# Optimization experiments

Measured on AMD Instinct MI355X. Metric: run time of the kernel, lower is better.

Reference implementation:

```python
import jax, jax.numpy as jnp
import numpy as np

N_FEATURES = 256
HIDDEN = 16
BATCH = 32768


def setup_inputs() -> dict:
    key = jax.random.key(0)
    ks = jax.random.split(key, 8)
    F, H = N_FEATURES, HIDDEN
    x = jax.random.normal(ks[0], (BATCH, F), dtype=jnp.float32)
    # Stacked per-feature subnet params (torch Linear: y = x @ W.T + b)
    s1 = 1.0  # fan_in=1 for fc1
    W1 = jax.random.uniform(ks[1], (F, H), minval=-s1, maxval=s1, dtype=jnp.float32)
    b1 = jax.random.uniform(ks[2], (F, H), minval=-s1, maxval=s1, dtype=jnp.float32)
    s2 = 1.0 / np.sqrt(H)
    W2 = jax.random.uniform(ks[3], (F, H, H), minval=-s2, maxval=s2, dtype=jnp.float32)  # [F, out, in]
    b2 = jax.random.uniform(ks[4], (F, H), minval=-s2, maxval=s2, dtype=jnp.float32)
    W3 = jax.random.uniform(ks[5], (F, H), minval=-s2, maxval=s2, dtype=jnp.float32)  # out=1
    b3 = jax.random.uniform(ks[6], (F,), minval=-s2, maxval=s2, dtype=jnp.float32)
    linear_a = jnp.zeros((F,), dtype=jnp.float32)
    bias_b = jnp.zeros((1,), dtype=jnp.float32)
    return {"x": x, "linear_a": linear_a, "bias_b": bias_b,
            "W1": W1, "b1": b1, "W2": W2, "b2": b2, "W3": W3, "b3": b3}


def reference(x, linear_a, bias_b, W1, b1, W2, b2, W3, b3):
    # lin term: (x * a).sum(1)
    lin = x @ linear_a  # [B]
    # all subnets batched: h1 [B, F, H]
    h1 = jax.nn.relu(x[:, :, None] * W1[None, :, :] + b1[None, :, :])
    # fc2: y = h1 @ W2.T per feature; W2 is [F, out, in]
    h2 = jax.nn.relu(jnp.einsum('bfh,fkh->bfk', h1, W2) + b2[None, :, :])
    # fc3 -> scalar per feature, then sum over features
    out_f = jnp.einsum('bfh,fh->bf', h2, W3) + b3[None, :]  # [B, F]
    add_sum = out_f.sum(axis=1)  # [B]
    logits = lin + bias_b[0] + add_sum
    return logits
```

## Files before the change

### kernel.cpp

```cpp
#include <hip/hip_runtime.h>


typedef float    f32x4 __attribute__((ext_vector_type(4)));
typedef _Float16 f16x4 __attribute__((ext_vector_type(4)));
typedef __fp16   pk16x2 __attribute__((ext_vector_type(2)));

__device__ __forceinline__ f16x4 cvt4(f32x4 v) {
    pk16x2 lo = __builtin_amdgcn_cvt_pkrtz(v[0], v[1]);
    pk16x2 hi = __builtin_amdgcn_cvt_pkrtz(v[2], v[3]);
    union { unsigned u[2]; f16x4 h; } un;
    un.u[0] = __builtin_bit_cast(unsigned, lo);
    un.u[1] = __builtin_bit_cast(unsigned, hi);
    return un.h;
}

__device__ __forceinline__ f16x4 relu_h(f16x4 v) {
    f16x4 z = {};
    return __builtin_elementwise_max(v, z);
}

__device__ __forceinline__ f32x4 relu_f(f32x4 v) {
    f32x4 z = {0.f, 0.f, 0.f, 0.f};
    return __builtin_elementwise_max(v, z);
}

#define FCHUNK 16
#define XR     20
#define W2R    20
#define BATCH  32768

__global__ __launch_bounds__(256) void igann_kernel(
    const float* __restrict__ x,  const float* __restrict__ la,
    const float* __restrict__ bb, const float* __restrict__ W1,
    const float* __restrict__ b1, const float* __restrict__ W2,
    const float* __restrict__ b2, const float* __restrict__ W3,
    const float* __restrict__ b3, float* __restrict__ ws)
{
    const int tid = threadIdx.x;
    const int l   = tid & 63;
    const int w   = tid >> 6;
    const int r   = l & 15;
    const int g   = l >> 4;
    const int g4  = g * 4;

    const int rb = blockIdx.x >> 4;
    const int fg = blockIdx.x & 15;
    const int f0 = fg * FCHUNK;
    const int rowbase = rb * 256;

    __shared__ _Float16 xs [256 * XR];
    __shared__ _Float16 w2s[FCHUNK * 16 * W2R];
    __shared__ _Float16 wbs[FCHUNK * 4 * 8];
    __shared__ float2   bws[FCHUNK * 16];
    __shared__ float    sums[256];

    {
        const int rr = tid >> 2;
        const int c4 = (tid & 3) * 4;
        #pragma unroll
        for (int it = 0; it < 4; ++it) {
            const int row = it * 64 + rr;
            f32x4 v = *(const f32x4*)(x + (size_t)(rowbase + row) * 256 + f0 + c4);
            *(f16x4*)(xs + row * XR + c4) = cvt4(v);
        }
    }
    {
        const int f = tid >> 4, n = tid & 15;
        const float* src = W2 + ((size_t)(f0 + f) * 16 + n) * 16;
        _Float16* dst = w2s + (f * 16 + n) * W2R;
        #pragma unroll
        for (int q = 0; q < 4; ++q) {
            f32x4 v = *(const f32x4*)(src + q * 4);
            *(f16x4*)(dst + q * 4) = cvt4(v);
        }
    }
    {
        const int f = tid >> 4, k = tid & 15;
        const int base = f * 32 + (k >> 2) * 8 + (k & 3);
        wbs[base]     = (_Float16)W1[(size_t)(f0 + f) * 16 + k];
        wbs[base + 4] = (_Float16)b1[(size_t)(f0 + f) * 16 + k];
    }
    {
        const int f = tid >> 4, n = tid & 15;
        bws[tid] = make_float2(b2[(size_t)(f0 + f) * 16 + n],
                               W3[(size_t)(f0 + f) * 16 + n]);
    }
    __syncthreads();

    const _Float16* xw = xs + (w * 64 + r) * XR;

    f32x4 acc[4];
    #pragma unroll
    for (int t = 0; t < 4; ++t) acc[t] = (f32x4){0.f, 0.f, 0.f, 0.f};

    for (int fi = 0; fi < FCHUNK; fi += 4) {
        f16x4 xv[4];
        #pragma unroll
        for (int t = 0; t < 4; ++t)
            xv[t] = *(const f16x4*)(xw + t * 16 * XR + fi);

        #pragma unroll
        for (int u = 0; u < 4; ++u) {
            const int f = fi + u;
            f16x4 w1h   = *(const f16x4*)(wbs + f * 32 + g * 8);
            f16x4 b1h   = *(const f16x4*)(wbs + f * 32 + g * 8 + 4);
            f16x4 bfrag = *(const f16x4*)(w2s + (f * 16 + r) * W2R + g4);
            const float2 bw = bws[f * 16 + r];
            const f32x4 cinit = {bw.x, bw.x, bw.x, bw.x};
            const f32x4 w3k4  = {bw.y, bw.y, bw.y, bw.y};

            #pragma unroll
            for (int t = 0; t < 4; ++t) {
                const _Float16 s = xv[t][u];
                f16x4 xb = {s, s, s, s};
                f16x4 h = relu_h(xb * w1h + b1h);
                f32x4 d = __builtin_amdgcn_mfma_f32_16x16x16f16(h, bfrag, cinit, 0, 0, 0);
                acc[t] += relu_f(d) * w3k4;
            }
        }
    }

    #pragma unroll
    for (int t = 0; t < 4; ++t)
        #pragma unroll
        for (int j = 0; j < 4; ++j) {
            float v = acc[t][j];
            v += __shfl_xor(v, 1, 64);
            v += __shfl_xor(v, 2, 64);
            v += __shfl_xor(v, 4, 64);
            v += __shfl_xor(v, 8, 64);
            if (r == 0)
                sums[w * 64 + t * 16 + g4 + j] = v;
        }
    __syncthreads();

    float b3s = 0.f;
    #pragma unroll
    for (int c = 0; c < FCHUNK; ++c) b3s += b3[f0 + c];
    float lin = 0.f;
    const _Float16* xrow = xs + tid * XR;
    #pragma unroll
    for (int c = 0; c < FCHUNK; ++c)
        lin = fmaf((float)xrow[c], la[f0 + c], lin);
    ws[(size_t)fg * BATCH + rowbase + tid] = sums[tid] + lin + b3s;
}

__global__ __launch_bounds__(256) void igann_reduce(
    const float* __restrict__ ws, const float* __restrict__ bb,
    float* __restrict__ out)
{
    const int i = blockIdx.x * 256 + threadIdx.x;
    float s = bb[0];
    #pragma unroll
    for (int gq = 0; gq < 16; ++gq)
        s += ws[(size_t)gq * BATCH + i];
    out[i] = s;
}

extern "C" void kernel_launch(void* const* d_in, const int* in_sizes, int n_in,
                              void* d_out, int out_size, void* d_ws, size_t ws_size,
                              hipStream_t stream) {
    const float* x  = (const float*)d_in[0];
    const float* la = (const float*)d_in[1];
    const float* bb = (const float*)d_in[2];
    const float* W1 = (const float*)d_in[3];
    const float* b1 = (const float*)d_in[4];
    const float* W2 = (const float*)d_in[5];
    const float* b2 = (const float*)d_in[6];
    const float* W3 = (const float*)d_in[7];
    const float* b3 = (const float*)d_in[8];
    float* out = (float*)d_out;
    float* ws  = (float*)d_ws;

    dim3 grid(2048), block(256);
    hipLaunchKernelGGL(igann_kernel, grid, block, 0, stream,
                       x, la, bb, W1, b1, W2, b2, W3, b3, ws);
    hipLaunchKernelGGL(igann_reduce, dim3(128), block, 0, stream,
                       ws, bb, out);
}
```

Measured before the change: 109.2 us.

## Swizzle LDS layouts, alias scratch buffers, and raise occupancy hint

Drops the padded shared-memory rows for x and W2 and uses an XOR swizzle on 4-element groups to avoid bank conflicts. This shrinks LDS use so more blocks fit per CU. The W1/b1 scratch is aliased with the reduction sums buffer, guarded by an added barrier. The launch bounds now ask for 8 waves-per-EU occupancy, and the accumulate uses an explicit FMA. The risks are extra address arithmetic and register pressure under the tighter occupancy bound.

```diff
diff --git a/kernel.cpp b/kernel.cpp
--- a/kernel.cpp
+++ b/kernel.cpp
@@ -25,11 +25,9 @@
 }
 
 #define FCHUNK 16
-#define XR     20
-#define W2R    20
 #define BATCH  32768
 
-__global__ __launch_bounds__(256) void igann_kernel(
+__global__ __launch_bounds__(256, 8) void igann_kernel(
     const float* __restrict__ x,  const float* __restrict__ la,
     const float* __restrict__ bb, const float* __restrict__ W1,
     const float* __restrict__ b1, const float* __restrict__ W2,
@@ -48,30 +46,33 @@
     const int f0 = fg * FCHUNK;
     const int rowbase = rb * 256;
 
-    __shared__ _Float16 xs [256 * XR];
-    __shared__ _Float16 w2s[FCHUNK * 16 * W2R];
-    __shared__ _Float16 wbs[FCHUNK * 4 * 8];
+    __shared__ _Float16 xs [256 * 16];
+    __shared__ _Float16 w2s[FCHUNK * 16 * 16];
+    __shared__ float    wbs_sums[256];
     __shared__ float2   bws[FCHUNK * 16];
-    __shared__ float    sums[256];
+    _Float16* wbs = (_Float16*)wbs_sums;
+    float*    sums = wbs_sums;
 
     {
-        const int rr = tid >> 2;
-        const int c4 = (tid & 3) * 4;
+        const int rr  = tid >> 2;
+        const int c4g = tid & 3;
+        const int sw  = (rr >> 2) & 3;
         #pragma unroll
         for (int it = 0; it < 4; ++it) {
             const int row = it * 64 + rr;
-            f32x4 v = *(const f32x4*)(x + (size_t)(rowbase + row) * 256 + f0 + c4);
-            *(f16x4*)(xs + row * XR + c4) = cvt4(v);
+            f32x4 v = *(const f32x4*)(x + (size_t)(rowbase + row) * 256 + f0 + c4g * 4);
+            *(f16x4*)(xs + row * 16 + ((c4g ^ sw) & 3) * 4) = cvt4(v);
         }
     }
     {
         const int f = tid >> 4, n = tid & 15;
+        const int sw = (n >> 2) & 3;
         const float* src = W2 + ((size_t)(f0 + f) * 16 + n) * 16;
-        _Float16* dst = w2s + (f * 16 + n) * W2R;
+        _Float16* dst = w2s + (f * 16 + n) * 16;
         #pragma unroll
         for (int q = 0; q < 4; ++q) {
             f32x4 v = *(const f32x4*)(src + q * 4);
-            *(f16x4*)(dst + q * 4) = cvt4(v);
+            *(f16x4*)(dst + ((q ^ sw) & 3) * 4) = cvt4(v);
         }
     }
     {
@@ -87,24 +88,27 @@
     }
     __syncthreads();
 
-    const _Float16* xw = xs + (w * 64 + r) * XR;
+    const _Float16* xw  = xs + (w * 64 + r) * 16;
+    const int       xsw = ((w * 64 + r) >> 2) & 3;
+    const _Float16* w2p = w2s + r * 16 + ((g ^ ((r >> 2) & 3)) & 3) * 4;
 
     f32x4 acc[4];
     #pragma unroll
     for (int t = 0; t < 4; ++t) acc[t] = (f32x4){0.f, 0.f, 0.f, 0.f};
 
     for (int fi = 0; fi < FCHUNK; fi += 4) {
+        const int xoff = (((fi >> 2) ^ xsw) & 3) * 4;
         f16x4 xv[4];
         #pragma unroll
         for (int t = 0; t < 4; ++t)
-            xv[t] = *(const f16x4*)(xw + t * 16 * XR + fi);
+            xv[t] = *(const f16x4*)(xw + t * 256 + xoff);
 
         #pragma unroll
         for (int u = 0; u < 4; ++u) {
             const int f = fi + u;
             f16x4 w1h   = *(const f16x4*)(wbs + f * 32 + g * 8);
             f16x4 b1h   = *(const f16x4*)(wbs + f * 32 + g * 8 + 4);
-            f16x4 bfrag = *(const f16x4*)(w2s + (f * 16 + r) * W2R + g4);
+            f16x4 bfrag = *(const f16x4*)(w2p + f * 256);
             const float2 bw = bws[f * 16 + r];
             const f32x4 cinit = {bw.x, bw.x, bw.x, bw.x};
             const f32x4 w3k4  = {bw.y, bw.y, bw.y, bw.y};
@@ -115,10 +119,12 @@
                 f16x4 xb = {s, s, s, s};
                 f16x4 h = relu_h(xb * w1h + b1h);
                 f32x4 d = __builtin_amdgcn_mfma_f32_16x16x16f16(h, bfrag, cinit, 0, 0, 0);
-                acc[t] += relu_f(d) * w3k4;
+                acc[t] = __builtin_elementwise_fma(relu_f(d), w3k4, acc[t]);
             }
         }
     }
+
+    __syncthreads();
 
     #pragma unroll
     for (int t = 0; t < 4; ++t)
@@ -138,10 +144,16 @@
     #pragma unroll
     for (int c = 0; c < FCHUNK; ++c) b3s += b3[f0 + c];
     float lin = 0.f;
-    const _Float16* xrow = xs + tid * XR;
-    #pragma unroll
-    for (int c = 0; c < FCHUNK; ++c)
-        lin = fmaf((float)xrow[c], la[f0 + c], lin);
+    {
+        const int swe = (tid >> 2) & 3;
+        #pragma unroll
+        for (int gq = 0; gq < 4; ++gq) {
+            f16x4 xv4 = *(const f16x4*)(xs + tid * 16 + ((gq ^ swe) & 3) * 4);
+            #pragma unroll
+            for (int e = 0; e < 4; ++e)
+                lin = fmaf((float)xv4[e], la[f0 + gq * 4 + e], lin);
+        }
+    }
     ws[(size_t)fg * BATCH + rowbase + tid] = sums[tid] + lin + b3s;
 }
 
```

New measurement: 106.6 us. -2.3%, faster.
